# Kernel optimization log

Measured on AMD Instinct MI355X. Metric: run time of the kernel, lower is better.

Reference implementation:

```python
import jax, jax.numpy as jnp
import numpy as np

N_NODES = 50000
N_EDGES = 800000
NFEAT, NHID, NCLASS, NCLUSTER = 512, 64, 16, 32


def gcn_conv(x, W, b, edge_index, edge_weight, n):
    """PyG GCNConv: add self-loops, symmetric normalization, linear + scatter-add."""
    row, col = edge_index[0], edge_index[1]
    loop = jnp.arange(n, dtype=row.dtype)
    row = jnp.concatenate([row, loop])
    col = jnp.concatenate([col, loop])
    w = jnp.concatenate([edge_weight, jnp.ones((n,), dtype=edge_weight.dtype)])
    # degree computed on target index (gcn_norm convention)
    deg = jax.ops.segment_sum(w, col, num_segments=n)
    dinv = jnp.where(deg > 0, jax.lax.rsqrt(deg), 0.0)
    norm = dinv[row] * w * dinv[col]          # [E+n]
    xw = x @ W                                # [n, out]
    msg = xw[row] * norm[:, None]             # gather + scale
    out = jax.ops.segment_sum(msg, col, num_segments=n)  # scatter-add
    return out + b


def setup_inputs() -> dict:
    key = jax.random.key(0)
    ks = jax.random.split(key, 12)
    def glorot(k, fan_in, fan_out):
        s = np.sqrt(6.0 / (fan_in + fan_out)).astype(np.float32)
        return jax.random.uniform(k, (fan_in, fan_out), jnp.float32, -s, s)
    x = jax.random.normal(ks[0], (N_NODES, NFEAT), jnp.float32)
    edge_index = jax.random.randint(ks[1], (2, N_EDGES), 0, N_NODES, dtype=jnp.int64)
    edge_weight = jax.random.uniform(ks[2], (N_EDGES,), jnp.float32)
    return {
        "x": x, "edge_index": edge_index, "edge_weight": edge_weight,
        "W1": glorot(ks[3], NFEAT, NHID), "b1": jnp.zeros((NHID,), jnp.float32),
        "W2": glorot(ks[4], NHID, NHID), "b2": jnp.zeros((NHID,), jnp.float32),
        "fcW1": glorot(ks[5], NHID, NCLASS), "fcb1": jnp.zeros((NCLASS,), jnp.float32),
        "fcW2": glorot(ks[6], NHID, NCLUSTER), "fcb2": jnp.zeros((NCLUSTER,), jnp.float32),
    }


def reference(x, edge_index, edge_weight, W1, b1, W2, b2, fcW1, fcb1, fcW2, fcb2):
    n = x.shape[0]
    h = jax.nn.relu(gcn_conv(x, W1, b1, edge_index, edge_weight, n))
    # dropout omitted (eval-mode / deterministic reference)
    h = gcn_conv(h, W2, b2, edge_index, edge_weight, n)
    pred = h @ fcW1 + fcb1
    pred_cluster = h @ fcW2 + fcb2
    return (pred, pred_cluster)
```

## Files before the change

### kernel.cpp

```cpp
#include <hip/hip_runtime.h>
#include <hip/hip_bf16.h>
#include <cstdint>
#include <cstddef>

#define N_FEAT 512
#define N_HID 64
#define N_CLASS 16
#define N_CLUSTER 32
#define NPART 8
#define KSPLIT 4

typedef short short8 __attribute__((ext_vector_type(8)));
typedef float floatx4 __attribute__((ext_vector_type(4)));
typedef unsigned short u16;
typedef unsigned short u16x4 __attribute__((ext_vector_type(4)));
typedef unsigned short u16x8 __attribute__((ext_vector_type(8)));

__device__ __forceinline__ short f2bf(float f) {
  __hip_bfloat16 h = __float2bfloat16(f);
  return *reinterpret_cast<short*>(&h);
}
__device__ __forceinline__ u16 f2bfu(float f) { return (u16)f2bf(f); }
__device__ __forceinline__ float bf2f(u16 u) {
  return __uint_as_float((unsigned)u << 16);
}

__global__ void k_zeroH(uint4* __restrict__ p, int n16) {
  int i = blockIdx.x * 256 + threadIdx.x;
  if (i < n16) p[i] = make_uint4(0u, 0u, 0u, 0u);
}

__global__ void k_degcnt2(const int* __restrict__ col, const float* __restrict__ w,
                          unsigned long long* __restrict__ hist, int H, int E) {
  int e = blockIdx.x * 256 + threadIdx.x;
  if (e >= E) return;
  int p = blockIdx.x & (NPART - 1);
  int c = col[e];
  unsigned long long fx = (unsigned long long)__float2uint_rn(w[e] * 16777216.0f);
  atomicAdd(&hist[(size_t)p * H + c], (1ull << 40) | fx);
}

__global__ __launch_bounds__(256) void k_redscan(
    const unsigned long long* __restrict__ hist, int H,
    float* __restrict__ dinv, int* __restrict__ off,
    int* __restrict__ bsum, int n) {
  __shared__ int sh[256];
  int t = threadIdx.x;
  int i = blockIdx.x * 256 + t;
  int v = 0;
  if (i < n) {
    unsigned long long tot = 0;
    #pragma unroll
    for (int p = 0; p < NPART; ++p) tot += hist[(size_t)p * H + i];
    v = (int)(tot >> 40);
    float wsum = (float)(tot & ((1ull << 40) - 1)) * 5.9604644775390625e-08f;
    dinv[i] = rsqrtf(1.0f + wsum);
  }
  sh[t] = v;
  __syncthreads();
  #pragma unroll
  for (int d = 1; d < 256; d <<= 1) {
    int x = 0;
    if (t >= d) x = sh[t - d];
    __syncthreads();
    if (t >= d) sh[t] += x;
    __syncthreads();
  }
  if (i < n) off[i] = sh[t] - v;
  if (t == 255) bsum[blockIdx.x] = sh[255];
}

__global__ __launch_bounds__(256) void k_scan2(const int* __restrict__ bsum,
                                               int* __restrict__ bsum2, int nb) {
  __shared__ int sh[256];
  int t = threadIdx.x;
  int v = (t < nb) ? bsum[t] : 0;
  sh[t] = v;
  __syncthreads();
  #pragma unroll
  for (int d = 1; d < 256; d <<= 1) {
    int x = 0;
    if (t >= d) x = sh[t - d];
    __syncthreads();
    if (t >= d) sh[t] += x;
    __syncthreads();
  }
  if (t < nb) bsum2[t] = sh[t] - v;
}

__global__ void k_scan3_initcur(int* __restrict__ off, const int* __restrict__ bsum2,
                                const unsigned long long* __restrict__ hist, int H,
                                int* __restrict__ cur, int n, int E) {
  int i = blockIdx.x * 256 + threadIdx.x;
  if (i < n) {
    int o = off[i] + bsum2[blockIdx.x];
    off[i] = o;
    int running = o;
    #pragma unroll
    for (int p = 0; p < NPART; ++p) {
      cur[(size_t)p * H + i] = running;
      running += (int)(hist[(size_t)p * H + i] >> 40);
    }
  }
  if (i == 0) off[n] = E;
}

__global__ void k_fill2(const int* __restrict__ rowi, const int* __restrict__ coli,
                        const float* __restrict__ w, const float* __restrict__ dinv,
                        int* __restrict__ cur, int H,
                        unsigned* __restrict__ pairs, int E) {
  int e = blockIdx.x * 256 + threadIdx.x;
  if (e >= E) return;
  int p = blockIdx.x & (NPART - 1);
  int r = rowi[e], c = coli[e];
  int pos = atomicAdd(&cur[(size_t)p * H + c], 1);
  pairs[pos] = ((unsigned)r << 16) | (u16)f2bf(dinv[r] * w[e] * dinv[c]);
}

__global__ void k_prepBF(const float* __restrict__ W, short* __restrict__ BF, int K) {
  int idx = blockIdx.x * 256 + threadIdx.x;
  int total = (K / 32) * 4 * 64;
  if (idx >= total) return;
  int lane = idx & 63;
  int sj = idx >> 6;
  int j = sj & 3, s = sj >> 2;
  int col = j * 16 + (lane & 15);
  int k0 = s * 32 + ((lane >> 4) << 3);
  short8 v;
  #pragma unroll
  for (int t = 0; t < 8; ++t) v[t] = f2bf(W[(size_t)(k0 + t) * 64 + col]);
  *(short8*)(BF + (size_t)idx * 8) = v;
}

__global__ __launch_bounds__(64, 5) void k_mfma128(
    const float* __restrict__ A, const short8* __restrict__ BF,
    u16* __restrict__ Cp, int M, int nbT) {
  const int q = blockIdx.x / nbT;
  const int tb = blockIdx.x - q * nbT;
  const int lane = threadIdx.x & 63;
  const int rbase = tb * 16;
  int r = rbase + (lane & 15);
  if (r >= M) r = M - 1;
  const float* arow = A + (size_t)r * 512 + q * 128 + ((lane >> 4) << 3);
  const short8* bbase = BF + q * 1024 + lane;

  float4 a[8];
  #pragma unroll
  for (int s = 0; s < 4; ++s) {
    a[2 * s]     = *(const float4*)(arow + s * 32);
    a[2 * s + 1] = *(const float4*)(arow + s * 32 + 4);
  }
  short8 pb[2][4];
  #pragma unroll
  for (int s = 0; s < 2; ++s)
    #pragma unroll
    for (int j = 0; j < 4; ++j)
      pb[s][j] = bbase[(s * 4 + j) * 64];
  __builtin_amdgcn_sched_barrier(0);

  floatx4 acc[4];
  #pragma unroll
  for (int j = 0; j < 4; ++j) acc[j] = (floatx4){0.f, 0.f, 0.f, 0.f};

  #pragma unroll
  for (int s = 0; s < 4; ++s) {
    const int sb = s & 1;
    float4 a0 = a[2 * s], a1 = a[2 * s + 1];
    short8 af;
    af[0] = f2bf(a0.x); af[1] = f2bf(a0.y); af[2] = f2bf(a0.z); af[3] = f2bf(a0.w);
    af[4] = f2bf(a1.x); af[5] = f2bf(a1.y); af[6] = f2bf(a1.z); af[7] = f2bf(a1.w);
    acc[0] = __builtin_amdgcn_mfma_f32_16x16x32_bf16(af, pb[sb][0], acc[0], 0, 0, 0);
    acc[1] = __builtin_amdgcn_mfma_f32_16x16x32_bf16(af, pb[sb][1], acc[1], 0, 0, 0);
    acc[2] = __builtin_amdgcn_mfma_f32_16x16x32_bf16(af, pb[sb][2], acc[2], 0, 0, 0);
    acc[3] = __builtin_amdgcn_mfma_f32_16x16x32_bf16(af, pb[sb][3], acc[3], 0, 0, 0);
    if (s + 2 < 4) {
      #pragma unroll
      for (int j = 0; j < 4; ++j)
        pb[sb][j] = bbase[((s + 2) * 4 + j) * 64];
    }
    __builtin_amdgcn_sched_barrier(0);
  }

  u16* Cq = Cp + (size_t)q * M * 64;
  const int srow = rbase + (lane >> 4) * 4;
  const int scol = lane & 15;
  #pragma unroll
  for (int i = 0; i < 4; ++i) {
    int rr = srow + i;
    if (rr < M) {
      #pragma unroll
      for (int j = 0; j < 4; ++j)
        Cq[(size_t)rr * 64 + j * 16 + scol] = f2bfu(acc[j][i]);
    }
  }
}

__global__ void k_comb(const u16* __restrict__ Cp, u16* __restrict__ Cf,
                       int n8, int part) {
  int i = blockIdx.x * 256 + threadIdx.x;
  if (i >= n8) return;
  u16x8 p0 = *(const u16x8*)(Cp + (size_t)i * 8);
  u16x8 p1 = *(const u16x8*)(Cp + (size_t)part + i * 8);
  u16x8 p2 = *(const u16x8*)(Cp + (size_t)2 * part + i * 8);
  u16x8 p3 = *(const u16x8*)(Cp + (size_t)3 * part + i * 8);
  u16x8 o;
  #pragma unroll
  for (int j = 0; j < 8; ++j)
    o[j] = f2bfu((bf2f(p0[j]) + bf2f(p1[j])) + (bf2f(p2[j]) + bf2f(p3[j])));
  *(u16x8*)(Cf + (size_t)i * 8) = o;
}

__global__ __launch_bounds__(64, 4) void k_mfma64(
    const u16* __restrict__ Av, const short8* __restrict__ BF,
    u16* __restrict__ C, int M) {
  const int lane = threadIdx.x & 63;
  const int rbase = blockIdx.x * 16;
  int r = rbase + (lane & 15);
  if (r >= M) r = M - 1;
  const int klo = (lane >> 4) * 8;
  const u16* arow = Av + (size_t)r * 64 + klo;
  const short8* bbase = BF + lane;

  short8 pah[2];
  short8 pb[2][4];
  pah[0] = *(const short8*)(arow);
  pah[1] = *(const short8*)(arow + 32);
  #pragma unroll
  for (int s = 0; s < 2; ++s)
    #pragma unroll
    for (int j = 0; j < 4; ++j)
      pb[s][j] = bbase[(s * 4 + j) * 64];

  floatx4 acc[4];
  #pragma unroll
  for (int j = 0; j < 4; ++j) acc[j] = (floatx4){0.f, 0.f, 0.f, 0.f};

  #pragma unroll
  for (int s = 0; s < 2; ++s) {
    acc[0] = __builtin_amdgcn_mfma_f32_16x16x32_bf16(pah[s], pb[s][0], acc[0], 0, 0, 0);
    acc[1] = __builtin_amdgcn_mfma_f32_16x16x32_bf16(pah[s], pb[s][1], acc[1], 0, 0, 0);
    acc[2] = __builtin_amdgcn_mfma_f32_16x16x32_bf16(pah[s], pb[s][2], acc[2], 0, 0, 0);
    acc[3] = __builtin_amdgcn_mfma_f32_16x16x32_bf16(pah[s], pb[s][3], acc[3], 0, 0, 0);
  }

  const int srow = rbase + (lane >> 4) * 4;
  const int scol = lane & 15;
  #pragma unroll
  for (int i = 0; i < 4; ++i) {
    int rr = srow + i;
    if (rr < M) {
      #pragma unroll
      for (int j = 0; j < 4; ++j)
        C[(size_t)rr * 64 + j * 16 + scol] = f2bfu(acc[j][i]);
    }
  }
}

template<bool RELU>
__global__ __launch_bounds__(256) void k_gather(
    const int* __restrict__ off, const unsigned* __restrict__ pairs,
    const float* __restrict__ dinv,
    const u16* __restrict__ xw, const float* __restrict__ bias,
    u16* __restrict__ h, int n) {
  int gid = blockIdx.x * 256 + threadIdx.x;
  int c = gid >> 6, lane = gid & 63;
  if (c >= n) return;
  float s = dinv[c]; s *= s;
  float acc = fmaf(bf2f(xw[(size_t)c * 64 + lane]), s, bias[lane]);
  int i = off[c], end = off[c + 1];
  for (; i + 7 < end; i += 8) {
    unsigned p[8];
    float v[8];
    #pragma unroll
    for (int t = 0; t < 8; ++t) p[t] = pairs[i + t];
    #pragma unroll
    for (int t = 0; t < 8; ++t)
      v[t] = bf2f(xw[(size_t)(p[t] >> 16) * 64 + lane]);
    #pragma unroll
    for (int t = 0; t < 8; ++t)
      acc = fmaf(v[t], __uint_as_float((p[t] & 0xffffu) << 16), acc);
  }
  for (; i + 1 < end; i += 2) {
    unsigned p0 = pairs[i], p1 = pairs[i + 1];
    float v0 = bf2f(xw[(size_t)(p0 >> 16) * 64 + lane]);
    float v1 = bf2f(xw[(size_t)(p1 >> 16) * 64 + lane]);
    acc = fmaf(v0, __uint_as_float((p0 & 0xffffu) << 16), acc);
    acc = fmaf(v1, __uint_as_float((p1 & 0xffffu) << 16), acc);
  }
  if (i < end) {
    unsigned p = pairs[i];
    acc = fmaf(bf2f(xw[(size_t)(p >> 16) * 64 + lane]),
               __uint_as_float((p & 0xffffu) << 16), acc);
  }
  if (RELU) acc = fmaxf(acc, 0.f);
  h[(size_t)c * 64 + lane] = f2bfu(acc);
}

__global__ __launch_bounds__(256) void k_fc(
    const u16* __restrict__ h,
    const float* __restrict__ fW1, const float* __restrict__ fb1,
    const float* __restrict__ fW2, const float* __restrict__ fb2,
    float* __restrict__ out, int M) {
  __shared__ float Hs[64][68];
  __shared__ float Ws[64][48];
  __shared__ float bs[48];
  const int t = threadIdx.x;
  const int row0 = blockIdx.x * 64;
  #pragma unroll
  for (int i = 0; i < 4; ++i) {
    int f = t + i * 256;
    int r = f >> 4, k4 = f & 15;
    int rr = row0 + r;
    float4 v = make_float4(0.f, 0.f, 0.f, 0.f);
    if (rr < M) {
      u16x4 u = *(const u16x4*)&h[(size_t)rr * 64 + k4 * 4];
      v = make_float4(bf2f(u[0]), bf2f(u[1]), bf2f(u[2]), bf2f(u[3]));
    }
    *(float4*)&Hs[r][k4 * 4] = v;
  }
  for (int f = t; f < 64 * 48; f += 256) {
    int k = f / 48, c = f - k * 48;
    Ws[k][c] = (c < 16) ? fW1[k * 16 + c] : fW2[k * 32 + (c - 16)];
  }
  if (t < 48) bs[t] = (t < 16) ? fb1[t] : fb2[t - 16];
  __syncthreads();
  const int tr = t >> 4, tc = t & 15;
  float acc[4][3] = {{0.f}};
  #pragma unroll 8
  for (int k = 0; k < 64; ++k) {
    float a[4], b[3];
    #pragma unroll
    for (int i = 0; i < 4; ++i) a[i] = Hs[tr * 4 + i][k];
    #pragma unroll
    for (int j = 0; j < 3; ++j) b[j] = Ws[k][tc * 3 + j];
    #pragma unroll
    for (int i = 0; i < 4; ++i)
      #pragma unroll
      for (int j = 0; j < 3; ++j) acc[i][j] = fmaf(a[i], b[j], acc[i][j]);
  }
  #pragma unroll
  for (int i = 0; i < 4; ++i) {
    int rr = row0 + tr * 4 + i;
    if (rr >= M) continue;
    #pragma unroll
    for (int j = 0; j < 3; ++j) {
      int c = tc * 3 + j;
      float v = acc[i][j] + bs[c];
      if (c < 16) out[(size_t)rr * 16 + c] = v;
      else out[(size_t)M * 16 + (size_t)rr * 32 + (c - 16)] = v;
    }
  }
}

extern "C" void kernel_launch(void* const* d_in, const int* in_sizes, int n_in,
                              void* d_out, int out_size, void* d_ws, size_t ws_size,
                              hipStream_t stream) {
  const float* x    = (const float*)d_in[0];
  const int*   ei   = (const int*)d_in[1];
  const float* ew   = (const float*)d_in[2];
  const float* W1   = (const float*)d_in[3];
  const float* b1   = (const float*)d_in[4];
  const float* W2   = (const float*)d_in[5];
  const float* b2   = (const float*)d_in[6];
  const float* fW1  = (const float*)d_in[7];
  const float* fb1  = (const float*)d_in[8];
  const float* fW2  = (const float*)d_in[9];
  const float* fb2  = (const float*)d_in[10];
  float* out = (float*)d_out;

  const int N = in_sizes[0] / N_FEAT;
  const int E = in_sizes[2];
  const int H = (N + 63) & ~63;
  const int* row = ei;
  const int* col = ei + E;

  char* ws = (char*)d_ws;
  float*              dinv = (float*)(ws + 0x000000);
  int*                off  = (int*)  (ws + 0x080000);
  int*                bsum = (int*)  (ws + 0x0C0000);
  int*                bsum2= (int*)  (ws + 0x0C1000);
  short*              BF1  = (short*)(ws + 0x0C8000);
  short*              BF2  = (short*)(ws + 0x0DA000);
  unsigned long long* hist = (unsigned long long*)(ws + 0x100000);
  int*                cur  = (int*)  (ws + 0x500000);
  unsigned*           pairs= (unsigned*)(ws + 0x6C0000);
  u16*                Cp   = (u16*)  (ws + 0xA00000);
  u16*                bufA = (u16*)  (ws + 0x2400000);
  u16*                bufB = (u16*)  (ws + 0x2B00000);

  const int nbN  = (N + 255) / 256;
  const int nbE  = (E + 255) / 256;
  const int nbT  = (N + 15) / 16;
  const int nbG  = (N + 63) / 64;
  const int nbW  = (N * 64 + 255) / 256;
  const int nH16 = NPART * H / 2;
  const int nbZ  = (nH16 + 255) / 256;
  const int n8   = N * 64 / 8;
  const int nbC  = (n8 + 255) / 256;

  k_prepBF<<<32, 256, 0, stream>>>(W1, BF1, N_FEAT);
  k_prepBF<<<2,  256, 0, stream>>>(W2, BF2, N_HID);

  k_zeroH  <<<nbZ, 256, 0, stream>>>((uint4*)hist, nH16);
  k_degcnt2<<<nbE, 256, 0, stream>>>(col, ew, hist, H, E);
  k_redscan<<<nbN, 256, 0, stream>>>(hist, H, dinv, off, bsum, N);
  k_scan2  <<<1,   256, 0, stream>>>(bsum, bsum2, nbN);
  k_scan3_initcur<<<nbN, 256, 0, stream>>>(off, bsum2, hist, H, cur, N, E);
  k_fill2  <<<nbE, 256, 0, stream>>>(row, col, ew, dinv, cur, H, pairs, E);

  k_mfma128<<<KSPLIT * nbT, 64, 0, stream>>>(x, (const short8*)BF1, Cp, N, nbT);
  k_comb   <<<nbC, 256, 0, stream>>>(Cp, bufA, n8, N * 64);
  k_gather<true><<<nbW, 256, 0, stream>>>(off, pairs, dinv, bufA, b1, bufB, N);

  k_mfma64<<<nbT, 64, 0, stream>>>(bufB, (const short8*)BF2, bufA, N);
  k_gather<false><<<nbW, 256, 0, stream>>>(off, pairs, dinv, bufA, b2, bufB, N);

  k_fc<<<nbG, 256, 0, stream>>>(bufB, fW1, fb1, fW2, fb2, out, N);
}
```

Baseline: 203.7 us.

## Fuse first-layer GEMM with CSR fill; drop K-split and combine pass

The first-layer GEMM no longer splits K four ways with bf16 partials and a separate combine kernel. Each wave now walks the full K=512 with a rolling prefetch of A rows and B fragments. The GEMM is launched in one kernel with the edge-fill (CSR bucketing) work, interleaving one GEMM block with four fill blocks, so the memory-bound streaming of x overlaps the atomic-heavy scatter. Weight prep and histogram zeroing are also merged into a single init launch. This removes two launches and the partial-buffer traffic, at the cost of fewer GEMM waves in flight and a longer serial K loop per wave.

```diff
diff --git a/kernel.cpp b/kernel.cpp
--- a/kernel.cpp
+++ b/kernel.cpp
@@ -8,13 +8,11 @@
 #define N_CLASS 16
 #define N_CLUSTER 32
 #define NPART 8
-#define KSPLIT 4
 
 typedef short short8 __attribute__((ext_vector_type(8)));
 typedef float floatx4 __attribute__((ext_vector_type(4)));
 typedef unsigned short u16;
 typedef unsigned short u16x4 __attribute__((ext_vector_type(4)));
-typedef unsigned short u16x8 __attribute__((ext_vector_type(8)));
 
 __device__ __forceinline__ short f2bf(float f) {
   __hip_bfloat16 h = __float2bfloat16(f);
@@ -25,9 +23,33 @@
   return __uint_as_float((unsigned)u << 16);
 }
 
-__global__ void k_zeroH(uint4* __restrict__ p, int n16) {
-  int i = blockIdx.x * 256 + threadIdx.x;
-  if (i < n16) p[i] = make_uint4(0u, 0u, 0u, 0u);
+__device__ __forceinline__ void prepBF_one(const float* __restrict__ W,
+                                           short* __restrict__ BF, int K, int idx) {
+  int lane = idx & 63;
+  int sj = idx >> 6;
+  int j = sj & 3, s = sj >> 2;
+  int col = j * 16 + (lane & 15);
+  int k0 = s * 32 + ((lane >> 4) << 3);
+  short8 v;
+  #pragma unroll
+  for (int t = 0; t < 8; ++t) v[t] = f2bf(W[(size_t)(k0 + t) * 64 + col]);
+  *(short8*)(BF + (size_t)idx * 8) = v;
+}
+
+__global__ void k_init(uint4* __restrict__ h16, int n16,
+                       const float* __restrict__ W1, short* __restrict__ BF1,
+                       const float* __restrict__ W2, short* __restrict__ BF2,
+                       int nbZ) {
+  int b = blockIdx.x, t = threadIdx.x;
+  if (b < nbZ) {
+    int i = b * 256 + t;
+    if (i < n16) h16[i] = make_uint4(0u, 0u, 0u, 0u);
+  } else if (b < nbZ + 16) {
+    prepBF_one(W1, BF1, N_FEAT, (b - nbZ) * 256 + t);
+  } else {
+    int idx = (b - nbZ - 16) * 256 + t;
+    if (idx < 512) prepBF_one(W2, BF2, N_HID, idx);
+  }
 }
 
 __global__ void k_degcnt2(const int* __restrict__ col, const float* __restrict__ w,
@@ -105,52 +127,23 @@
   if (i == 0) off[n] = E;
 }
 
-__global__ void k_fill2(const int* __restrict__ rowi, const int* __restrict__ coli,
-                        const float* __restrict__ w, const float* __restrict__ dinv,
-                        int* __restrict__ cur, int H,
-                        unsigned* __restrict__ pairs, int E) {
-  int e = blockIdx.x * 256 + threadIdx.x;
-  if (e >= E) return;
-  int p = blockIdx.x & (NPART - 1);
-  int r = rowi[e], c = coli[e];
-  int pos = atomicAdd(&cur[(size_t)p * H + c], 1);
-  pairs[pos] = ((unsigned)r << 16) | (u16)f2bf(dinv[r] * w[e] * dinv[c]);
-}
-
-__global__ void k_prepBF(const float* __restrict__ W, short* __restrict__ BF, int K) {
-  int idx = blockIdx.x * 256 + threadIdx.x;
-  int total = (K / 32) * 4 * 64;
-  if (idx >= total) return;
-  int lane = idx & 63;
-  int sj = idx >> 6;
-  int j = sj & 3, s = sj >> 2;
-  int col = j * 16 + (lane & 15);
-  int k0 = s * 32 + ((lane >> 4) << 3);
-  short8 v;
-  #pragma unroll
-  for (int t = 0; t < 8; ++t) v[t] = f2bf(W[(size_t)(k0 + t) * 64 + col]);
-  *(short8*)(BF + (size_t)idx * 8) = v;
-}
-
-__global__ __launch_bounds__(64, 5) void k_mfma128(
+__device__ __forceinline__ void gemm_wave(
     const float* __restrict__ A, const short8* __restrict__ BF,
-    u16* __restrict__ Cp, int M, int nbT) {
-  const int q = blockIdx.x / nbT;
-  const int tb = blockIdx.x - q * nbT;
+    u16* __restrict__ C, int M, int tile) {
   const int lane = threadIdx.x & 63;
-  const int rbase = tb * 16;
+  const int rbase = tile * 16;
   int r = rbase + (lane & 15);
   if (r >= M) r = M - 1;
-  const float* arow = A + (size_t)r * 512 + q * 128 + ((lane >> 4) << 3);
-  const short8* bbase = BF + q * 1024 + lane;
-
-  float4 a[8];
+  const float* arow = A + (size_t)r * 512 + ((lane >> 4) << 3);
+  const short8* bbase = BF + lane;
+
+  float4 pa0[4], pa1[4];
+  short8 pb[2][4];
   #pragma unroll
   for (int s = 0; s < 4; ++s) {
-    a[2 * s]     = *(const float4*)(arow + s * 32);
-    a[2 * s + 1] = *(const float4*)(arow + s * 32 + 4);
-  }
-  short8 pb[2][4];
+    pa0[s] = *(const float4*)(arow + s * 32);
+    pa1[s] = *(const float4*)(arow + s * 32 + 4);
+  }
   #pragma unroll
   for (int s = 0; s < 2; ++s)
     #pragma unroll
@@ -163,9 +156,10 @@
   for (int j = 0; j < 4; ++j) acc[j] = (floatx4){0.f, 0.f, 0.f, 0.f};
 
   #pragma unroll
-  for (int s = 0; s < 4; ++s) {
+  for (int s = 0; s < 16; ++s) {
+    const int sa = s & 3;
     const int sb = s & 1;
-    float4 a0 = a[2 * s], a1 = a[2 * s + 1];
+    float4 a0 = pa0[sa], a1 = pa1[sa];
     short8 af;
     af[0] = f2bf(a0.x); af[1] = f2bf(a0.y); af[2] = f2bf(a0.z); af[3] = f2bf(a0.w);
     af[4] = f2bf(a1.x); af[5] = f2bf(a1.y); af[6] = f2bf(a1.z); af[7] = f2bf(a1.w);
@@ -173,7 +167,11 @@
     acc[1] = __builtin_amdgcn_mfma_f32_16x16x32_bf16(af, pb[sb][1], acc[1], 0, 0, 0);
     acc[2] = __builtin_amdgcn_mfma_f32_16x16x32_bf16(af, pb[sb][2], acc[2], 0, 0, 0);
     acc[3] = __builtin_amdgcn_mfma_f32_16x16x32_bf16(af, pb[sb][3], acc[3], 0, 0, 0);
-    if (s + 2 < 4) {
+    if (s + 4 < 16) {
+      pa0[sa] = *(const float4*)(arow + (s + 4) * 32);
+      pa1[sa] = *(const float4*)(arow + (s + 4) * 32 + 4);
+    }
+    if (s + 2 < 16) {
       #pragma unroll
       for (int j = 0; j < 4; ++j)
         pb[sb][j] = bbase[((s + 2) * 4 + j) * 64];
@@ -181,7 +179,6 @@
     __builtin_amdgcn_sched_barrier(0);
   }
 
-  u16* Cq = Cp + (size_t)q * M * 64;
   const int srow = rbase + (lane >> 4) * 4;
   const int scol = lane & 15;
   #pragma unroll
@@ -190,24 +187,37 @@
     if (rr < M) {
       #pragma unroll
       for (int j = 0; j < 4; ++j)
-        Cq[(size_t)rr * 64 + j * 16 + scol] = f2bfu(acc[j][i]);
-    }
-  }
-}
-
-__global__ void k_comb(const u16* __restrict__ Cp, u16* __restrict__ Cf,
-                       int n8, int part) {
-  int i = blockIdx.x * 256 + threadIdx.x;
-  if (i >= n8) return;
-  u16x8 p0 = *(const u16x8*)(Cp + (size_t)i * 8);
-  u16x8 p1 = *(const u16x8*)(Cp + (size_t)part + i * 8);
-  u16x8 p2 = *(const u16x8*)(Cp + (size_t)2 * part + i * 8);
-  u16x8 p3 = *(const u16x8*)(Cp + (size_t)3 * part + i * 8);
-  u16x8 o;
-  #pragma unroll
-  for (int j = 0; j < 8; ++j)
-    o[j] = f2bfu((bf2f(p0[j]) + bf2f(p1[j])) + (bf2f(p2[j]) + bf2f(p3[j])));
-  *(u16x8*)(Cf + (size_t)i * 8) = o;
+        C[(size_t)rr * 64 + j * 16 + scol] = f2bfu(acc[j][i]);
+    }
+  }
+}
+
+__device__ __forceinline__ void fill_block(
+    int f, const int* __restrict__ rowi, const int* __restrict__ coli,
+    const float* __restrict__ w, const float* __restrict__ dinv,
+    int* __restrict__ cur, int H, unsigned* __restrict__ pairs, int E) {
+  int e = f * 256 + threadIdx.x;
+  if (e >= E) return;
+  int p = f & (NPART - 1);
+  int r = rowi[e], c = coli[e];
+  int pos = atomicAdd(&cur[(size_t)p * H + c], 1);
+  pairs[pos] = ((unsigned)r << 16) | (u16)f2bf(dinv[r] * w[e] * dinv[c]);
+}
+
+__global__ __launch_bounds__(256, 4) void k_gemmfill(
+    const float* __restrict__ A, const short8* __restrict__ BF,
+    u16* __restrict__ C, int M, int nbT,
+    const int* __restrict__ rowi, const int* __restrict__ coli,
+    const float* __restrict__ w, const float* __restrict__ dinv,
+    int* __restrict__ cur, int H, unsigned* __restrict__ pairs, int E) {
+  const int q = blockIdx.x / 5;
+  const int r = blockIdx.x % 5;
+  if (r == 0) {
+    int tile = q * 4 + (threadIdx.x >> 6);
+    if (tile < nbT) gemm_wave(A, BF, C, M, tile);
+  } else {
+    fill_block(q * 4 + (r - 1), rowi, coli, w, dinv, cur, H, pairs, E);
+  }
 }
 
 __global__ __launch_bounds__(64, 4) void k_mfma64(
@@ -384,32 +394,29 @@
   unsigned long long* hist = (unsigned long long*)(ws + 0x100000);
   int*                cur  = (int*)  (ws + 0x500000);
   unsigned*           pairs= (unsigned*)(ws + 0x6C0000);
-  u16*                Cp   = (u16*)  (ws + 0xA00000);
-  u16*                bufA = (u16*)  (ws + 0x2400000);
-  u16*                bufB = (u16*)  (ws + 0x2B00000);
+  u16*                bufA = (u16*)  (ws + 0xD40000);
+  u16*                bufB = (u16*)  (ws + 0x1980000);
 
   const int nbN  = (N + 255) / 256;
   const int nbE  = (E + 255) / 256;
   const int nbT  = (N + 15) / 16;
+  const int nGB  = (nbT + 3) / 4;
   const int nbG  = (N + 63) / 64;
   const int nbW  = (N * 64 + 255) / 256;
   const int nH16 = NPART * H / 2;
   const int nbZ  = (nH16 + 255) / 256;
-  const int n8   = N * 64 / 8;
-  const int nbC  = (n8 + 255) / 256;
-
-  k_prepBF<<<32, 256, 0, stream>>>(W1, BF1, N_FEAT);
-  k_prepBF<<<2,  256, 0, stream>>>(W2, BF2, N_HID);
-
-  k_zeroH  <<<nbZ, 256, 0, stream>>>((uint4*)hist, nH16);
+
+  k_init<<<nbZ + 18, 256, 0, stream>>>((uint4*)hist, nH16, W1, BF1, W2, BF2, nbZ);
+
   k_degcnt2<<<nbE, 256, 0, stream>>>(col, ew, hist, H, E);
   k_redscan<<<nbN, 256, 0, stream>>>(hist, H, dinv, off, bsum, N);
   k_scan2  <<<1,   256, 0, stream>>>(bsum, bsum2, nbN);
   k_scan3_initcur<<<nbN, 256, 0, stream>>>(off, bsum2, hist, H, cur, N, E);
-  k_fill2  <<<nbE, 256, 0, stream>>>(row, col, ew, dinv, cur, H, pairs, E);
-
-  k_mfma128<<<KSPLIT * nbT, 64, 0, stream>>>(x, (const short8*)BF1, Cp, N, nbT);
-  k_comb   <<<nbC, 256, 0, stream>>>(Cp, bufA, n8, N * 64);
+
+  k_gemmfill<<<5 * nGB, 256, 0, stream>>>(
+      x, (const short8*)BF1, bufA, N, nbT,
+      row, col, ew, dinv, cur, H, pairs, E);
+
   k_gather<true><<<nbW, 256, 0, stream>>>(off, pairs, dinv, bufA, b1, bufB, N);
 
   k_mfma64<<<nbT, 64, 0, stream>>>(bufB, (const short8*)BF2, bufA, N);
```

Result: faster. 188.8 us (-7.3%).
